# Optimization experiments

Hardware: AMD Instinct MI355X
Metric: run time of the kernel (lower is better)

The kernel has to match this reference:

```python
import jax, jax.numpy as jnp
import numpy as np

N_NODES = 100000
N_EDGES = 1600000
D_IN = 128
D_OUT = 128


def setup_inputs() -> dict:
    key = jax.random.key(0)
    k1, k2, k3, k4 = jax.random.split(key, 4)
    x = jax.random.normal(k1, (N_NODES, D_IN), dtype=jnp.float32)
    # Xavier-uniform-like init for weight (exact distribution irrelevant for correctness baseline)
    weight = jax.random.normal(k2, (D_IN, D_OUT), dtype=jnp.float32) * (1.0 / np.sqrt(D_IN))
    bias = jnp.zeros((D_OUT,), dtype=jnp.float32)
    edge_index = jax.random.randint(k3, (2, N_EDGES), 0, N_NODES, dtype=jnp.int64 if jax.config.read('jax_enable_x64') else jnp.int32)
    edge_weight = jax.random.uniform(k4, (N_EDGES,), dtype=jnp.float32)
    return {"x": x, "weight": weight, "bias": bias,
            "edge_index": edge_index, "edge_weight": edge_weight}


def reference(x, weight, bias, edge_index, edge_weight):
    # support = X @ W   -- dense projection [N, D_out]
    support = x @ weight
    # output = A @ support -- SpMM via gather + weighted segment-sum
    src = edge_index[1]  # column index of adj (neighbor being aggregated)
    dst = edge_index[0]  # row index of adj (node receiving the message)
    messages = support[src] * edge_weight[:, None]          # [E, D_out]
    out = jax.ops.segment_sum(messages, dst, num_segments=N_NODES)  # [N, D_out]
    return out + bias
```

## Files before the change

### kernel.cpp

```cpp
#include <hip/hip_runtime.h>
#include <hip/hip_bf16.h>

#define N_NODES 100000
#define N_EDGES 1600000
#define D 128

#define NBUK 1024
#define BSH 7
#define NAGG ((N_NODES + 127) >> BSH)
#define CAP 2560
#define PA_BLOCKS 256
#define PA_EPB 6250
#define SRC_MASK 0x01FFFFFF

typedef __attribute__((ext_vector_type(8))) short bf16x8;
typedef __attribute__((ext_vector_type(4))) float f32x4;

static __device__ __forceinline__ short f2bf(float f) {
    unsigned u = __builtin_bit_cast(unsigned, f);
    u += 0x7FFFu + ((u >> 16) & 1u);
    return (short)(u >> 16);
}
static __device__ __forceinline__ float bf2f(unsigned short h) {
    unsigned u = ((unsigned)h) << 16;
    return __builtin_bit_cast(float, u);
}

__global__ void wt_kernel(const float* __restrict__ w, short* __restrict__ wt) {
    const int i = blockIdx.x * blockDim.x + threadIdx.x;
    if (i < D * D) {
        const int k = i / D, c = i % D;
        wt[c * D + k] = f2bf(w[i]);
    }
}

__global__ __launch_bounds__(256) void gemm_mfma_kernel(
    const float* __restrict__ x, const short* __restrict__ wt,
    short* __restrict__ sup) {
    const int wid = blockIdx.x * 4 + (threadIdx.x >> 6);
    if (wid >= N_NODES / 16) return;
    const int l = threadIdx.x & 63;
    const int r = l & 15, g = l >> 4;
    const size_t row0 = (size_t)wid * 16;

    bf16x8 a[4];
    const float* xp = x + (row0 + r) * D + g * 8;
#pragma unroll
    for (int ks = 0; ks < 4; ++ks) {
        const float4 f0 = *reinterpret_cast<const float4*>(xp + ks * 32);
        const float4 f1 = *reinterpret_cast<const float4*>(xp + ks * 32 + 4);
        bf16x8 t;
        t[0] = f2bf(f0.x); t[1] = f2bf(f0.y); t[2] = f2bf(f0.z); t[3] = f2bf(f0.w);
        t[4] = f2bf(f1.x); t[5] = f2bf(f1.y); t[6] = f2bf(f1.z); t[7] = f2bf(f1.w);
        a[ks] = t;
    }

#pragma unroll
    for (int nt = 0; nt < 8; ++nt) {
        f32x4 acc = {0.f, 0.f, 0.f, 0.f};
        const short* wp = wt + (size_t)(nt * 16 + r) * D + g * 8;
#pragma unroll
        for (int ks = 0; ks < 4; ++ks) {
            const bf16x8 b = *reinterpret_cast<const bf16x8*>(wp + ks * 32);
            acc = __builtin_amdgcn_mfma_f32_16x16x32_bf16(a[ks], b, acc, 0, 0, 0);
        }
        short* sp = sup + (row0 + g * 4) * D + nt * 16 + r;
#pragma unroll
        for (int q = 0; q < 4; ++q) sp[q * D] = f2bf(acc[q]);
    }
}

__global__ __launch_bounds__(1024) void bukscatter_kernel(
    const int* __restrict__ dst, const int* __restrict__ src,
    const float* __restrict__ ew, int* __restrict__ gcur,
    int2* __restrict__ inter_sw) {
    __shared__ int h[NBUK];
    const int t = threadIdx.x;
    if (t < NBUK) h[t] = 0;
    __syncthreads();
    const int beg = blockIdx.x * PA_EPB;
    const int end = min(beg + PA_EPB, N_EDGES);
    for (int i = beg + t; i < end; i += 1024)
        atomicAdd(&h[dst[i] >> BSH], 1);
    __syncthreads();
    if (t < NBUK) {
        const int c = h[t];
        h[t] = c ? (t * CAP + atomicAdd(&gcur[t], c)) : 0;
    }
    __syncthreads();
    for (int i = beg + t; i < end; i += 1024) {
        const int d = dst[i];
        const int pos = atomicAdd(&h[d >> BSH], 1);
        inter_sw[pos] = make_int2(src[i] | ((d & 127) << 25), __float_as_int(ew[i]));
    }
}

__global__ __launch_bounds__(512) void sortagg_kernel(
    const int* __restrict__ gcur, const int2* __restrict__ inter_sw,
    const short* __restrict__ sup, const float* __restrict__ bias,
    float* __restrict__ out) {
    __shared__ int2 eb[CAP];
    __shared__ int st[128];
    __shared__ int cur[128];
    const int b = blockIdx.x, t = threadIdx.x;
    const int cnt = gcur[b];
    const int2* in = inter_sw + (size_t)b * CAP;

    if (t < 128) st[t] = 0;
    __syncthreads();

    int2 e0, e1, e2, e3, e4;
    const int i0 = t, i1 = t + 512, i2 = t + 1024, i3 = t + 1536, i4 = t + 2048;
    if (i0 < cnt) { e0 = in[i0]; atomicAdd(&st[(unsigned)e0.x >> 25], 1); }
    if (i1 < cnt) { e1 = in[i1]; atomicAdd(&st[(unsigned)e1.x >> 25], 1); }
    if (i2 < cnt) { e2 = in[i2]; atomicAdd(&st[(unsigned)e2.x >> 25], 1); }
    if (i3 < cnt) { e3 = in[i3]; atomicAdd(&st[(unsigned)e3.x >> 25], 1); }
    if (i4 < cnt) { e4 = in[i4]; atomicAdd(&st[(unsigned)e4.x >> 25], 1); }
    __syncthreads();

    int hv = 0;
    if (t < 128) { hv = st[t]; cur[t] = hv; }
    __syncthreads();
    for (int o = 1; o < 128; o <<= 1) {
        int v = 0;
        if (t < 128 && t >= o) v = cur[t - o];
        __syncthreads();
        if (t < 128) cur[t] += v;
        __syncthreads();
    }
    if (t < 128) {
        const int s = cur[t] - hv;
        st[t] = s;
        cur[t] = s;
    }
    __syncthreads();

    if (i0 < cnt) eb[atomicAdd(&cur[(unsigned)e0.x >> 25], 1)] = make_int2(e0.x & SRC_MASK, e0.y);
    if (i1 < cnt) eb[atomicAdd(&cur[(unsigned)e1.x >> 25], 1)] = make_int2(e1.x & SRC_MASK, e1.y);
    if (i2 < cnt) eb[atomicAdd(&cur[(unsigned)e2.x >> 25], 1)] = make_int2(e2.x & SRC_MASK, e2.y);
    if (i3 < cnt) eb[atomicAdd(&cur[(unsigned)e3.x >> 25], 1)] = make_int2(e3.x & SRC_MASK, e3.y);
    if (i4 < cnt) eb[atomicAdd(&cur[(unsigned)e4.x >> 25], 1)] = make_int2(e4.x & SRC_MASK, e4.y);
    __syncthreads();

    const int wv = t >> 6, lane = t & 63;
    const int g = lane >> 4;
    const int fl = lane & 15;

    const float4 b0 = *reinterpret_cast<const float4*>(&bias[fl * 8]);
    const float4 b1 = *reinterpret_cast<const float4*>(&bias[fl * 8 + 4]);

    for (int k = 0; k < 16; ++k) {
        const int nl = wv * 16 + k;
        const int node = (b << BSH) + nl;
        if (node >= N_NODES) break;
        const int beg = st[nl], end = cur[nl];

        float acc[8] = {0, 0, 0, 0, 0, 0, 0, 0};
        for (int i = beg + g; i < end; i += 4) {
            const int2 sw = eb[i];
            const float w = __int_as_float(sw.y);
            const bf16x8 v = *reinterpret_cast<const bf16x8*>(
                &sup[(size_t)sw.x * D + fl * 8]);
#pragma unroll
            for (int q = 0; q < 8; ++q)
                acc[q] = fmaf(w, bf2f((unsigned short)v[q]), acc[q]);
        }
#pragma unroll
        for (int q = 0; q < 8; ++q) {
            acc[q] += __shfl_xor(acc[q], 16);
            acc[q] += __shfl_xor(acc[q], 32);
        }
        if (g == 0) {
            float* o = &out[(size_t)node * D + fl * 8];
            reinterpret_cast<float4*>(o)[0] =
                make_float4(acc[0] + b0.x, acc[1] + b0.y, acc[2] + b0.z, acc[3] + b0.w);
            reinterpret_cast<float4*>(o)[1] =
                make_float4(acc[4] + b1.x, acc[5] + b1.y, acc[6] + b1.z, acc[7] + b1.w);
        }
    }
}

extern "C" void kernel_launch(void* const* d_in, const int* in_sizes, int n_in,
                              void* d_out, int out_size, void* d_ws, size_t ws_size,
                              hipStream_t stream) {
    const float* x      = (const float*)d_in[0];
    const float* weight = (const float*)d_in[1];
    const float* bias   = (const float*)d_in[2];
    const int*   eidx   = (const int*)d_in[3];
    const float* ew     = (const float*)d_in[4];
    float* out = (float*)d_out;

    const int* dst_idx = eidx;
    const int* src_idx = eidx + N_EDGES;

    char* p = (char*)d_ws;
    short* sup       = (short*)p;  p += (size_t)N_NODES * D * 2;
    short* wt        = (short*)p;  p += (size_t)D * D * 2;
    int*   gcur      = (int*)p;    p += NBUK * 4;
    int2*  inter_sw  = (int2*)p;   p += (size_t)NBUK * CAP * 8;

    wt_kernel<<<(D * D + 255) / 256, 256, 0, stream>>>(weight, wt);
    hipMemsetAsync(gcur, 0, (size_t)NBUK * 4, stream);
    gemm_mfma_kernel<<<(N_NODES / 16 + 3) / 4, 256, 0, stream>>>(x, wt, sup);

    bukscatter_kernel<<<PA_BLOCKS, 1024, 0, stream>>>(dst_idx, src_idx, ew, gcur,
                                                      inter_sw);

    sortagg_kernel<<<NAGG, 512, 0, stream>>>(gcur, inter_sw, sup, bias, out);
}
```

Before: 136.4 us.

## Fuse GEMM with edge bucket scatter and widen per-lane aggregation to 16 features

```diff
diff --git a/kernel.cpp b/kernel.cpp
--- a/kernel.cpp
+++ b/kernel.cpp
@@ -9,8 +9,9 @@
 #define BSH 7
 #define NAGG ((N_NODES + 127) >> BSH)
 #define CAP 2560
-#define PA_BLOCKS 256
+#define NSCAT 256
 #define PA_EPB 6250
+#define NGB ((N_NODES / 16 + 15) / 16)
 #define SRC_MASK 0x01FFFFFF
 
 typedef __attribute__((ext_vector_type(8))) short bf16x8;
@@ -26,20 +27,49 @@
     return __builtin_bit_cast(float, u);
 }
 
-__global__ void wt_kernel(const float* __restrict__ w, short* __restrict__ wt) {
+__global__ void wt_kernel(const float* __restrict__ w, short* __restrict__ wt,
+                          int* __restrict__ gcur) {
     const int i = blockIdx.x * blockDim.x + threadIdx.x;
     if (i < D * D) {
         const int k = i / D, c = i % D;
         wt[c * D + k] = f2bf(w[i]);
     }
-}
-
-__global__ __launch_bounds__(256) void gemm_mfma_kernel(
+    if (i < NBUK) gcur[i] = 0;
+}
+
+__global__ __launch_bounds__(1024, 8) void gemm_scatter_kernel(
     const float* __restrict__ x, const short* __restrict__ wt,
-    short* __restrict__ sup) {
-    const int wid = blockIdx.x * 4 + (threadIdx.x >> 6);
+    short* __restrict__ sup, const int* __restrict__ dst,
+    const int* __restrict__ src, const float* __restrict__ ew,
+    int* __restrict__ gcur, int2* __restrict__ inter_sw) {
+    __shared__ int h[NBUK];
+    const int t = threadIdx.x;
+
+    if (blockIdx.x < NSCAT) {
+        if (t < NBUK) h[t] = 0;
+        __syncthreads();
+        const int beg = blockIdx.x * PA_EPB;
+        const int end = min(beg + PA_EPB, N_EDGES);
+        for (int i = beg + t; i < end; i += 1024)
+            atomicAdd(&h[dst[i] >> BSH], 1);
+        __syncthreads();
+        if (t < NBUK) {
+            const int c = h[t];
+            h[t] = c ? (t * CAP + atomicAdd(&gcur[t], c)) : 0;
+        }
+        __syncthreads();
+        for (int i = beg + t; i < end; i += 1024) {
+            const int d = dst[i];
+            const int pos = atomicAdd(&h[d >> BSH], 1);
+            inter_sw[pos] = make_int2(src[i] | ((d & 127) << 25),
+                                      __float_as_int(ew[i]));
+        }
+        return;
+    }
+
+    const int wid = (blockIdx.x - NSCAT) * 16 + (t >> 6);
     if (wid >= N_NODES / 16) return;
-    const int l = threadIdx.x & 63;
+    const int l = t & 63;
     const int r = l & 15, g = l >> 4;
     const size_t row0 = (size_t)wid * 16;
 
@@ -49,10 +79,10 @@
     for (int ks = 0; ks < 4; ++ks) {
         const float4 f0 = *reinterpret_cast<const float4*>(xp + ks * 32);
         const float4 f1 = *reinterpret_cast<const float4*>(xp + ks * 32 + 4);
-        bf16x8 t;
-        t[0] = f2bf(f0.x); t[1] = f2bf(f0.y); t[2] = f2bf(f0.z); t[3] = f2bf(f0.w);
-        t[4] = f2bf(f1.x); t[5] = f2bf(f1.y); t[6] = f2bf(f1.z); t[7] = f2bf(f1.w);
-        a[ks] = t;
+        bf16x8 tt;
+        tt[0] = f2bf(f0.x); tt[1] = f2bf(f0.y); tt[2] = f2bf(f0.z); tt[3] = f2bf(f0.w);
+        tt[4] = f2bf(f1.x); tt[5] = f2bf(f1.y); tt[6] = f2bf(f1.z); tt[7] = f2bf(f1.w);
+        a[ks] = tt;
     }
 
 #pragma unroll
@@ -67,31 +97,6 @@
         short* sp = sup + (row0 + g * 4) * D + nt * 16 + r;
 #pragma unroll
         for (int q = 0; q < 4; ++q) sp[q * D] = f2bf(acc[q]);
-    }
-}
-
-__global__ __launch_bounds__(1024) void bukscatter_kernel(
-    const int* __restrict__ dst, const int* __restrict__ src,
-    const float* __restrict__ ew, int* __restrict__ gcur,
-    int2* __restrict__ inter_sw) {
-    __shared__ int h[NBUK];
-    const int t = threadIdx.x;
-    if (t < NBUK) h[t] = 0;
-    __syncthreads();
-    const int beg = blockIdx.x * PA_EPB;
-    const int end = min(beg + PA_EPB, N_EDGES);
-    for (int i = beg + t; i < end; i += 1024)
-        atomicAdd(&h[dst[i] >> BSH], 1);
-    __syncthreads();
-    if (t < NBUK) {
-        const int c = h[t];
-        h[t] = c ? (t * CAP + atomicAdd(&gcur[t], c)) : 0;
-    }
-    __syncthreads();
-    for (int i = beg + t; i < end; i += 1024) {
-        const int d = dst[i];
-        const int pos = atomicAdd(&h[d >> BSH], 1);
-        inter_sw[pos] = make_int2(src[i] | ((d & 127) << 25), __float_as_int(ew[i]));
     }
 }
 
@@ -143,39 +148,52 @@
     __syncthreads();
 
     const int wv = t >> 6, lane = t & 63;
-    const int g = lane >> 4;
-    const int fl = lane & 15;
-
-    const float4 b0 = *reinterpret_cast<const float4*>(&bias[fl * 8]);
-    const float4 b1 = *reinterpret_cast<const float4*>(&bias[fl * 8 + 4]);
+    const int g = lane >> 3;
+    const int fl = lane & 7;
+
+    const float4 b0 = *reinterpret_cast<const float4*>(&bias[fl * 16]);
+    const float4 b1 = *reinterpret_cast<const float4*>(&bias[fl * 16 + 4]);
+    const float4 b2 = *reinterpret_cast<const float4*>(&bias[fl * 16 + 8]);
+    const float4 b3 = *reinterpret_cast<const float4*>(&bias[fl * 16 + 12]);
 
     for (int k = 0; k < 16; ++k) {
         const int nl = wv * 16 + k;
         const int node = (b << BSH) + nl;
         if (node >= N_NODES) break;
-        const int beg = st[nl], end = cur[nl];
-
-        float acc[8] = {0, 0, 0, 0, 0, 0, 0, 0};
-        for (int i = beg + g; i < end; i += 4) {
+        const int end = cur[nl];
+
+        float acc[16];
+#pragma unroll
+        for (int q = 0; q < 16; ++q) acc[q] = 0.f;
+
+        for (int i = st[nl] + g; i < end; i += 8) {
             const int2 sw = eb[i];
             const float w = __int_as_float(sw.y);
-            const bf16x8 v = *reinterpret_cast<const bf16x8*>(
-                &sup[(size_t)sw.x * D + fl * 8]);
-#pragma unroll
-            for (int q = 0; q < 8; ++q)
-                acc[q] = fmaf(w, bf2f((unsigned short)v[q]), acc[q]);
-        }
-#pragma unroll
-        for (int q = 0; q < 8; ++q) {
+            const short* rp = &sup[(size_t)sw.x * D + fl * 16];
+            const bf16x8 v0 = *reinterpret_cast<const bf16x8*>(rp);
+            const bf16x8 v1 = *reinterpret_cast<const bf16x8*>(rp + 8);
+#pragma unroll
+            for (int q = 0; q < 8; ++q) {
+                acc[q] = fmaf(w, bf2f((unsigned short)v0[q]), acc[q]);
+                acc[8 + q] = fmaf(w, bf2f((unsigned short)v1[q]), acc[8 + q]);
+            }
+        }
+#pragma unroll
+        for (int q = 0; q < 16; ++q) {
+            acc[q] += __shfl_xor(acc[q], 8);
             acc[q] += __shfl_xor(acc[q], 16);
             acc[q] += __shfl_xor(acc[q], 32);
         }
         if (g == 0) {
-            float* o = &out[(size_t)node * D + fl * 8];
+            float* o = &out[(size_t)node * D + fl * 16];
             reinterpret_cast<float4*>(o)[0] =
                 make_float4(acc[0] + b0.x, acc[1] + b0.y, acc[2] + b0.z, acc[3] + b0.w);
             reinterpret_cast<float4*>(o)[1] =
                 make_float4(acc[4] + b1.x, acc[5] + b1.y, acc[6] + b1.z, acc[7] + b1.w);
+            reinterpret_cast<float4*>(o)[2] =
+                make_float4(acc[8] + b2.x, acc[9] + b2.y, acc[10] + b2.z, acc[11] + b2.w);
+            reinterpret_cast<float4*>(o)[3] =
+                make_float4(acc[12] + b3.x, acc[13] + b3.y, acc[14] + b3.z, acc[15] + b3.w);
         }
     }
 }
@@ -199,12 +217,10 @@
     int*   gcur      = (int*)p;    p += NBUK * 4;
     int2*  inter_sw  = (int2*)p;   p += (size_t)NBUK * CAP * 8;
 
-    wt_kernel<<<(D * D + 255) / 256, 256, 0, stream>>>(weight, wt);
-    hipMemsetAsync(gcur, 0, (size_t)NBUK * 4, stream);
-    gemm_mfma_kernel<<<(N_NODES / 16 + 3) / 4, 256, 0, stream>>>(x, wt, sup);
-
-    bukscatter_kernel<<<PA_BLOCKS, 1024, 0, stream>>>(dst_idx, src_idx, ew, gcur,
-                                                      inter_sw);
+    wt_kernel<<<(D * D + 255) / 256, 256, 0, stream>>>(weight, wt, gcur);
+
+    gemm_scatter_kernel<<<NSCAT + NGB, 1024, 0, stream>>>(
+        x, wt, sup, dst_idx, src_idx, ew, gcur, inter_sw);
 
     sortagg_kernel<<<NAGG, 512, 0, stream>>>(gcur, inter_sw, sup, bias, out);
 }
```

Result: slower. 151.5 us (+11.1%).
